# Kernel tuning notes

Measured on AMD Instinct MI355X. Metric: run time of the kernel, lower is better.

## Reference

```python
import jax, jax.numpy as jnp
import numpy as np

N_NODES = 100000
N_EDGES = 1600000
IN_FEATS = 256
N_HIDDEN = 128
N_CLASSES = 40


def setup_inputs() -> dict:
    key = jax.random.key(0)
    k1, k2, k3, k4, k5 = jax.random.split(key, 5)
    features = jax.random.normal(k1, (N_NODES, IN_FEATS), dtype=jnp.float32)
    edge_src = jax.random.randint(k2, (N_EDGES,), 0, N_NODES, dtype=jnp.int64)
    edge_dst = jax.random.randint(k3, (N_EDGES,), 0, N_NODES, dtype=jnp.int64)
    # GraphConv weights (Glorot-ish scaling)
    W1 = jax.random.normal(k4, (IN_FEATS, N_HIDDEN), dtype=jnp.float32) / np.sqrt(IN_FEATS)
    b1 = jnp.zeros((N_HIDDEN,), dtype=jnp.float32)
    W2 = jax.random.normal(k5, (N_HIDDEN, N_CLASSES), dtype=jnp.float32) / np.sqrt(N_HIDDEN)
    b2 = jnpspace = None
    b2 = jnp.zeros((N_CLASSES,), dtype=jnp.float32)
    return {"features": features, "edge_src": edge_src, "edge_dst": edge_dst,
            "W1": W1, "b1": b1, "W2": W2, "b2": b2}


def _degree_norms(edge_src, edge_dst, n_nodes):
    ones = jnp.ones(edge_src.shape[0], dtype=jnp.float32)
    deg_out = jax.ops.segment_sum(ones, edge_src, num_segments=n_nodes)
    deg_in = jax.ops.segment_sum(ones, edge_dst, num_segments=n_nodes)
    norm_src = jax.lax.rsqrt(jnp.clip(deg_out, 1.0))  # D_out^{-1/2}
    norm_dst = jax.lax.rsqrt(jnp.clip(deg_in, 1.0))   # D_in^{-1/2}
    return norm_src, norm_dst


def _graph_conv(x, W, b, edge_src, edge_dst, norm_src, norm_dst, activation=None):
    # DGL GraphConv norm='both': out = D_in^{-1/2} A D_out^{-1/2} (x W) + b
    h = (x @ W) * norm_src[:, None]                       # transform then src-normalize
    agg = jax.ops.segment_sum(h[edge_src], edge_dst,
                              num_segments=x.shape[0])    # sparse neighbor aggregation
    out = agg * norm_dst[:, None] + b
    if activation is not None:
        out = activation(out)
    return out


def reference(features, edge_src, edge_dst, W1, b1, W2, b2):
    norm_src, norm_dst = _degree_norms(edge_src, edge_dst, features.shape[0])
    h = _graph_conv(features, W1, b1, edge_src, edge_dst, norm_src, norm_dst,
                    activation=jax.nn.relu)
    # dropout is identity in eval-mode reference
    out = _graph_conv(h, W2, b2, edge_src, edge_dst, norm_src, norm_dst)
    return out
```

## Files before the change

### kernel.cpp

```cpp
#include <hip/hip_runtime.h>
#include <hip/hip_bf16.h>
#include <hip/hip_fp16.h>

#define NN 100000
#define NE 1600000
#define KF 256
#define NH 128
#define NC 40
#define PAD 64
#define CMAX 63

#define NBLK_P 512
#define PCHUNK (NE / NBLK_P)
#define BUK 256
#define NBUK ((NN + BUK - 1) / BUK)
#define CAP 6144


__device__ __forceinline__ float ldf(const void* p, size_t i, bool bf){
  return bf ? __bfloat162float(((const __hip_bfloat16*)p)[i]) : ((const float*)p)[i];
}
__device__ __forceinline__ void cv2(unsigned int v, float* o){
  union { unsigned int i; float f; } a, b;
  a.i = v << 16; b.i = v & 0xffff0000u;
  o[0] = a.f; o[1] = b.f;
}

__global__ void k_sniff_edges(const unsigned int* __restrict__ e, unsigned int* __restrict__ flags){
  __shared__ unsigned int sh[256];
  unsigned int v = 0;
  for (int i = blockIdx.x * 256 + threadIdx.x; i < NE / 2; i += gridDim.x * 256)
    v |= e[2 * i + 1];
  sh[threadIdx.x] = v;
  __syncthreads();
  for (int off = 128; off; off >>= 1){
    if (threadIdx.x < off) sh[threadIdx.x] |= sh[threadIdx.x + off];
    __syncthreads();
  }
  if (threadIdx.x == 0 && sh[0]) atomicOr(&flags[0], sh[0]);
}

__global__ void k_sniff_float(const unsigned int* __restrict__ w, unsigned int* __restrict__ flags){
  __shared__ unsigned int sh[256];
  unsigned int hits = 0;
  for (int i = blockIdx.x * 256 + threadIdx.x; i < (1 << 20); i += gridDim.x * 256){
    unsigned int b = (w[i] >> 7) & 0xFFu;
    hits += (b >= 118u && b <= 130u) ? 1u : 0u;
  }
  sh[threadIdx.x] = hits;
  __syncthreads();
  for (int off = 128; off; off >>= 1){
    if (threadIdx.x < off) sh[threadIdx.x] += sh[threadIdx.x + off];
    __syncthreads();
  }
  if (threadIdx.x == 0) atomicAdd(&flags[1], sh[0]);
}

__device__ __forceinline__ int edge_at(const void* p, int e, bool is64){
  return is64 ? (int)((const long long*)p)[e] : ((const int*)p)[e];
}
__device__ __forceinline__ bool f_isbf(const unsigned int* flags){ return flags[1] > (1u << 19); }

__global__ __launch_bounds__(256) void k_part(const void* __restrict__ src,
    const void* __restrict__ dst, const unsigned int* __restrict__ flags,
    int* __restrict__ deg_out, int* __restrict__ gcur, unsigned int* __restrict__ part){
  __shared__ int cnt[NBUK];
  __shared__ int base[NBUK];
  const bool is64 = (flags[0] == 0u);
  const int beg = blockIdx.x * PCHUNK;
  const int end = min(beg + PCHUNK, NE);
  for (int t = threadIdx.x; t < NBUK; t += 256) cnt[t] = 0;
  __syncthreads();
  for (int e = beg + threadIdx.x; e < end; e += 256){
    int d = edge_at(dst, e, is64);
    atomicAdd(&cnt[d >> 8], 1);
  }
  __syncthreads();
  for (int t = threadIdx.x; t < NBUK; t += 256){
    int c = cnt[t];
    base[t] = c ? atomicAdd(&gcur[t], c) : 0;
    cnt[t] = 0;
  }
  __syncthreads();
  for (int e = beg + threadIdx.x; e < end; e += 256){
    int d = edge_at(dst, e, is64);
    int s = edge_at(src, e, is64);
    atomicAdd(&deg_out[s], 1);
    int b = d >> 8;
    int pos = base[b] + atomicAdd(&cnt[b], 1);
    if (pos < CAP)
      part[(size_t)b * CAP + pos] = ((unsigned int)s << 8) | (unsigned int)(d & 255);
  }
}

__global__ __launch_bounds__(256) void k_csr(const unsigned int* __restrict__ part,
    const int* __restrict__ gcur, int* __restrict__ fill, int* __restrict__ csr_pad){
  __shared__ int rows[256 * CMAX];
  __shared__ int fl[256];
  const int b = blockIdx.x;
  fl[threadIdx.x] = 0;
  __syncthreads();
  const int n = min(gcur[b], CAP);
  for (int i = threadIdx.x; i < n; i += 256){
    unsigned int e = part[(size_t)b * CAP + i];
    int r = (int)(e & 255u);
    int s = (int)(e >> 8);
    int pos = atomicAdd(&fl[r], 1);
    if (pos < CMAX) rows[r * CMAX + pos] = s;
  }
  __syncthreads();
  const int node0 = b * BUK;
  if (node0 + threadIdx.x < NN) fill[node0 + threadIdx.x] = fl[threadIdx.x];
  for (int idx = threadIdx.x; idx < 256 * CMAX; idx += 256){
    int r = idx / CMAX;
    int c = idx - r * CMAX;
    int node = node0 + r;
    if (node < NN) csr_pad[node * PAD + c] = rows[idx];
  }
}

__global__ void k_norms(const int* __restrict__ deg_out, const int* __restrict__ fill,
                        float* __restrict__ nsrc, float* __restrict__ ndst){
  int i = blockIdx.x * 256 + threadIdx.x;
  if (i < NN){
    nsrc[i] = rsqrtf(fmaxf((float)deg_out[i], 1.f));
    ndst[i] = rsqrtf(fmaxf((float)fill[i], 1.f));
  }
}

__global__ __launch_bounds__(256) void k_gemm1(const void* __restrict__ feat,
    const void* __restrict__ W1, const unsigned int* __restrict__ flags,
    const float* __restrict__ nsrc, __half* __restrict__ h1){
  const bool isbf = f_isbf(flags);
  __shared__ float As[64][68];
  __shared__ float Bs[64][128];
  const int t = threadIdx.x;
  const int row0 = blockIdx.x * 64;
  const int cg = t & 15;
  const int rg = t >> 4;
  float acc[4][8];
  #pragma unroll
  for (int i = 0; i < 4; i++)
    #pragma unroll
    for (int j = 0; j < 8; j++) acc[i][j] = 0.f;

  const int ar   = t >> 2;
  const int ak   = (t & 3) * 16;
  const int arow = row0 + ar;

  for (int kc = 0; kc < KF; kc += 64){
    if (arow < NN){
      size_t off = (size_t)arow * KF + kc + ak;
      if (isbf){
        const uint4* p = (const uint4*)((const __hip_bfloat16*)feat + off);
        uint4 u0 = p[0], u1 = p[1];
        float tmp[16];
        cv2(u0.x, tmp+0);  cv2(u0.y, tmp+2);  cv2(u0.z, tmp+4);  cv2(u0.w, tmp+6);
        cv2(u1.x, tmp+8);  cv2(u1.y, tmp+10); cv2(u1.z, tmp+12); cv2(u1.w, tmp+14);
        #pragma unroll
        for (int j = 0; j < 16; j++) As[ar][ak + j] = tmp[j];
      } else {
        const float4* p = (const float4*)((const float*)feat + off);
        float4 v0 = p[0], v1 = p[1], v2 = p[2], v3 = p[3];
        *(float4*)&As[ar][ak +  0] = v0;
        *(float4*)&As[ar][ak +  4] = v1;
        *(float4*)&As[ar][ak +  8] = v2;
        *(float4*)&As[ar][ak + 12] = v3;
      }
    } else {
      #pragma unroll
      for (int j = 0; j < 16; j++) As[ar][ak + j] = 0.f;
    }
    if (isbf){
      #pragma unroll
      for (int q0 = 0; q0 < 4; q0++){
        int q  = t + q0 * 256;
        int bk = q >> 4;
        int bc = (q & 15) * 8;
        uint4 u = *(const uint4*)((const __hip_bfloat16*)W1 + (size_t)(kc + bk) * NH + bc);
        float tmp[8];
        cv2(u.x, tmp); cv2(u.y, tmp+2); cv2(u.z, tmp+4); cv2(u.w, tmp+6);
        #pragma unroll
        for (int j = 0; j < 8; j++) Bs[bk][bc + j] = tmp[j];
      }
    } else {
      #pragma unroll
      for (int q0 = 0; q0 < 8; q0++){
        int q  = t + q0 * 256;
        int bk = q >> 5;
        int bc = (q & 31) * 4;
        *(float4*)&Bs[bk][bc] = *(const float4*)((const float*)W1 + (size_t)(kc + bk) * NH + bc);
      }
    }
    __syncthreads();
    #pragma unroll 8
    for (int k = 0; k < 64; k++){
      float a0 = As[rg*4+0][k];
      float a1 = As[rg*4+1][k];
      float a2 = As[rg*4+2][k];
      float a3 = As[rg*4+3][k];
      float b[8];
      #pragma unroll
      for (int j = 0; j < 8; j++) b[j] = Bs[k][cg*8 + j];
      #pragma unroll
      for (int j = 0; j < 8; j++){
        acc[0][j] += a0 * b[j];
        acc[1][j] += a1 * b[j];
        acc[2][j] += a2 * b[j];
        acc[3][j] += a3 * b[j];
      }
    }
    __syncthreads();
  }
  #pragma unroll
  for (int i = 0; i < 4; i++){
    int r = row0 + rg*4 + i;
    if (r < NN){
      float s = nsrc[r];
      __half2* op = (__half2*)(h1 + (size_t)r * NH) + cg*4;
      #pragma unroll
      for (int j = 0; j < 4; j++)
        op[j] = __floats2half2_rn(acc[i][2*j] * s, acc[i][2*j+1] * s);
    }
  }
}

__global__ __launch_bounds__(256) void k_agg1(const int* __restrict__ csr_pad,
    const int* __restrict__ fill, const float* __restrict__ ndst,
    const unsigned int* __restrict__ h1w, const void* __restrict__ b1,
    const unsigned int* __restrict__ flags, float* __restrict__ x1){
  const bool isbf = f_isbf(flags);
  int node = blockIdx.x * 4 + (threadIdx.x >> 6);
  if (node >= NN) return;
  int lane = threadIdx.x & 63;
  int beg = node * PAD;
  int end = beg + min(fill[node], CMAX);
  float ax0 = 0.f, ay0 = 0.f, ax1 = 0.f, ay1 = 0.f;
  int e = beg;
  for (; e + 2 <= end; e += 2){
    int s0 = csr_pad[e], s1 = csr_pad[e+1];
    unsigned int u0 = h1w[(size_t)s0 * (NH/2) + lane];
    unsigned int u1 = h1w[(size_t)s1 * (NH/2) + lane];
    float2 v0 = __half22float2(*(__half2*)&u0);
    float2 v1 = __half22float2(*(__half2*)&u1);
    ax0 += v0.x; ay0 += v0.y;
    ax1 += v1.x; ay1 += v1.y;
  }
  if (e < end){
    int s0 = csr_pad[e];
    unsigned int u0 = h1w[(size_t)s0 * (NH/2) + lane];
    float2 v0 = __half22float2(*(__half2*)&u0);
    ax0 += v0.x; ay0 += v0.y;
  }
  float nd = ndst[node];
  float bx = ldf(b1, lane*2,   isbf);
  float by = ldf(b1, lane*2+1, isbf);
  float2 o;
  o.x = fmaxf((ax0 + ax1) * nd + bx, 0.f);
  o.y = fmaxf((ay0 + ay1) * nd + by, 0.f);
  ((float2*)(x1 + (size_t)node * NH))[lane] = o;
}

__global__ __launch_bounds__(256) void k_gemm2(const float* __restrict__ x1,
    const void* __restrict__ W2, const unsigned int* __restrict__ flags,
    const float* __restrict__ nsrc, __half* __restrict__ h2){
  const bool isbf = f_isbf(flags);
  __shared__ float Xs[128][68];
  __shared__ float Ws[64][44];
  const int t = threadIdx.x;
  const int row0 = blockIdx.x * 128;
  const int cg = t & 7;
  const int rg = t >> 3;
  float acc[4][5];
  #pragma unroll
  for (int i = 0; i < 4; i++)
    #pragma unroll
    for (int j = 0; j < 5; j++) acc[i][j] = 0.f;

  for (int kc = 0; kc < NH; kc += 64){
    #pragma unroll
    for (int q0 = 0; q0 < 8; q0++){
      int q  = t + q0 * 256;
      int r  = q >> 4;
      int kq = (q & 15) * 4;
      int grow = row0 + r;
      float4 v;
      if (grow < NN) v = *(const float4*)(x1 + (size_t)grow * NH + kc + kq);
      else { v.x = v.y = v.z = v.w = 0.f; }
      *(float4*)&Xs[r][kq] = v;
    }
    #pragma unroll
    for (int q0 = 0; q0 < 10; q0++){
      int idx = t + q0 * 256;
      int k = idx / 40;
      int c = idx - k * 40;
      Ws[k][c] = ldf(W2, (size_t)(kc + k) * NC + c, isbf);
    }
    __syncthreads();
    #pragma unroll 4
    for (int k = 0; k < 64; k++){
      float a0 = Xs[rg*4+0][k];
      float a1 = Xs[rg*4+1][k];
      float a2 = Xs[rg*4+2][k];
      float a3 = Xs[rg*4+3][k];
      float b[5];
      #pragma unroll
      for (int j = 0; j < 5; j++) b[j] = Ws[k][cg*5 + j];
      #pragma unroll
      for (int j = 0; j < 5; j++){
        acc[0][j] += a0 * b[j];
        acc[1][j] += a1 * b[j];
        acc[2][j] += a2 * b[j];
        acc[3][j] += a3 * b[j];
      }
    }
    __syncthreads();
  }
  #pragma unroll
  for (int i = 0; i < 4; i++){
    int r = row0 + rg*4 + i;
    if (r < NN){
      float s = nsrc[r];
      #pragma unroll
      for (int j = 0; j < 5; j++)
        h2[(size_t)r * NC + cg*5 + j] = __float2half_rn(acc[i][j] * s);
    }
  }
}

__global__ __launch_bounds__(256) void k_agg2(const int* __restrict__ csr_pad,
    const int* __restrict__ fill, const float* __restrict__ ndst,
    const unsigned int* __restrict__ h2w, const void* __restrict__ b2,
    const unsigned int* __restrict__ flags, float* __restrict__ out){
  const bool isbf = f_isbf(flags);
  int node = blockIdx.x * 4 + (threadIdx.x >> 6);
  if (node >= NN) return;
  int lane = threadIdx.x & 63;
  int beg = node * PAD;
  int end = beg + min(fill[node], CMAX);
  if (lane < NC/2){
    float ax0 = 0.f, ay0 = 0.f, ax1 = 0.f, ay1 = 0.f;
    int e = beg;
    for (; e + 2 <= end; e += 2){
      int s0 = csr_pad[e], s1 = csr_pad[e+1];
      unsigned int u0 = h2w[(size_t)s0 * (NC/2) + lane];
      unsigned int u1 = h2w[(size_t)s1 * (NC/2) + lane];
      float2 v0 = __half22float2(*(__half2*)&u0);
      float2 v1 = __half22float2(*(__half2*)&u1);
      ax0 += v0.x; ay0 += v0.y;
      ax1 += v1.x; ay1 += v1.y;
    }
    if (e < end){
      int s0 = csr_pad[e];
      unsigned int u0 = h2w[(size_t)s0 * (NC/2) + lane];
      float2 v0 = __half22float2(*(__half2*)&u0);
      ax0 += v0.x; ay0 += v0.y;
    }
    float nd = ndst[node];
    float2 o;
    o.x = (ax0 + ax1) * nd + ldf(b2, 2*lane,   isbf);
    o.y = (ay0 + ay1) * nd + ldf(b2, 2*lane+1, isbf);
    ((float2*)(out + (size_t)node * NC))[lane] = o;
  }
}

extern "C" void kernel_launch(void* const* d_in, const int* in_sizes, int n_in,
                              void* d_out, int out_size, void* d_ws, size_t ws_size,
                              hipStream_t stream) {
  const long long SZ_FEAT = (long long)NN * KF, SZ_E = NE, SZ_W1 = (long long)KF * NH,
                  SZ_B1 = NH, SZ_W2 = (long long)NH * NC, SZ_B2 = NC;
  int i_feat = -1, i_e1 = -1, i_e2 = -1, i_W1 = -1, i_b1 = -1, i_W2 = -1, i_b2 = -1;
  auto m = [](long long s, long long z){ return s == z || s == 4*z || s == 8*z || s == 2*z; };
  for (int i = 0; i < n_in; i++){
    long long s = in_sizes[i];
    if      (m(s, SZ_FEAT)) i_feat = i;
    else if (m(s, SZ_E))    { if (i_e1 < 0) i_e1 = i; else i_e2 = i; }
    else if (m(s, SZ_W1))   i_W1 = i;
    else if (m(s, SZ_B1))   i_b1 = i;
    else if (m(s, SZ_W2))   i_W2 = i;
    else if (m(s, SZ_B2))   i_b2 = i;
  }
  if (i_feat < 0 || i_e2 < 0 || i_W1 < 0 || i_b1 < 0 || i_W2 < 0 || i_b2 < 0){
    i_feat = 0; i_e1 = 1; i_e2 = 2; i_W1 = 3; i_b1 = 4; i_W2 = 5; i_b2 = 6;
  }
  const void* feat = d_in[i_feat];
  const void* esrc = d_in[i_e1];
  const void* edst = d_in[i_e2];
  const void* W1   = d_in[i_W1];
  const void* b1   = d_in[i_b1];
  const void* W2   = d_in[i_W2];
  const void* b2   = d_in[i_b2];
  float* out = (float*)d_out;

  int* deg_out        = (int*)d_ws;
  int* fill           = deg_out + NN;
  unsigned int* flags = (unsigned int*)(fill + NN);
  int* gcur           = (int*)(flags + 4);
  float* norm_src     = (float*)(gcur + 400);
  float* norm_dst     = norm_src + NN;
  int* csr_pad        = (int*)(norm_dst + NN);
  __half* h1          = (__half*)(csr_pad + (size_t)NN * PAD);
  float* x1           = (float*)(h1 + (size_t)NN * NH);
  __half* h2          = h1;
  unsigned int* part  = (unsigned int*)x1;

  hipMemsetAsync(deg_out, 0, ((size_t)2 * NN + 4 + 400) * sizeof(int), stream);

  k_sniff_edges<<<400, 256, 0, stream>>>((const unsigned int*)esrc, flags);
  k_sniff_float<<<256, 256, 0, stream>>>((const unsigned int*)feat, flags);
  k_part<<<NBLK_P, 256, 0, stream>>>(esrc, edst, flags, deg_out, gcur, part);
  k_csr <<<NBUK,   256, 0, stream>>>(part, gcur, fill, csr_pad);
  k_norms<<<(NN + 255) / 256, 256, 0, stream>>>(deg_out, fill, norm_src, norm_dst);

  k_gemm1<<<(NN + 63) / 64, 256, 0, stream>>>(feat, W1, flags, norm_src, h1);
  k_agg1 <<<(NN + 3) / 4, 256, 0, stream>>>(csr_pad, fill, norm_dst,
                                            (const unsigned int*)h1, b1, flags, x1);
  k_gemm2<<<(NN + 127) / 128, 256, 0, stream>>>(x1, W2, flags, norm_src, h2);
  k_agg2 <<<(NN + 3) / 4, 256, 0, stream>>>(csr_pad, fill, norm_dst,
                                            (const unsigned int*)h2, b2, flags, out);
}
```

Measured before the change: 599.6 us.

## Add bf16 MFMA path for first-layer GEMM with pre-swizzled weights

Adds a kernel that rearranges W1 into per-lane bf16x8 fragments, plus a new GEMM1 kernel that uses 16x16x32 bf16 MFMA instructions when the inputs are detected as bf16. The old shared-memory scalar GEMM1 now handles only the fp32 case. The aim is to replace scalar FMA work and bf16-to-float conversion with matrix-core instructions. The cost is two extra kernel launches: the weight swizzle, and whichever GEMM kernel exits early for the other dtype.

Result: no change. 594.2 us (-0.9%).

```diff
diff --git a/kernel.cpp b/kernel.cpp
--- a/kernel.cpp
+++ b/kernel.cpp
@@ -15,6 +15,9 @@
 #define BUK 256
 #define NBUK ((NN + BUK - 1) / BUK)
 #define CAP 6144
+
+typedef __attribute__((ext_vector_type(8))) short bf16x8;
+typedef __attribute__((ext_vector_type(4))) float f32x4;
 
 
 __device__ __forceinline__ float ldf(const void* p, size_t i, bool bf){
@@ -128,10 +131,68 @@
   }
 }
 
+__global__ void k_w1s(const void* __restrict__ W1, const unsigned int* __restrict__ flags,
+                      bf16x8* __restrict__ w1s){
+  if (!f_isbf(flags)) return;
+  int idx = blockIdx.x * 256 + threadIdx.x;
+  if (idx >= 4096) return;
+  int l    = idx & 63;
+  int tile = idx >> 6;
+  int kt   = tile >> 3;
+  int nt   = tile & 7;
+  int krow = kt * 32 + (l >> 4) * 8;
+  int col  = nt * 16 + (l & 15);
+  const unsigned short* w = (const unsigned short*)W1;
+  bf16x8 v;
+  #pragma unroll
+  for (int j = 0; j < 8; j++)
+    v[j] = (short)w[(size_t)(krow + j) * NH + col];
+  w1s[idx] = v;
+}
+
+__global__ __launch_bounds__(256) void k_gemm1_mfma(const void* __restrict__ feat,
+    const bf16x8* __restrict__ w1s, const unsigned int* __restrict__ flags,
+    const float* __restrict__ nsrc, __half* __restrict__ h1){
+  if (!f_isbf(flags)) return;
+  const int t  = threadIdx.x;
+  const int wv = t >> 6;
+  const int l  = t & 63;
+  const int row0 = blockIdx.x * 64 + wv * 16;
+  const int arow = row0 + (l & 15);
+  const short* fp = (const short*)feat;
+  const size_t abase = (size_t)min(arow, NN - 1) * KF + (l >> 4) * 8;
+
+  f32x4 acc[8];
+  #pragma unroll
+  for (int n = 0; n < 8; n++) acc[n] = (f32x4){0.f, 0.f, 0.f, 0.f};
+
+  #pragma unroll 2
+  for (int kt = 0; kt < 8; kt++){
+    bf16x8 a = *(const bf16x8*)(fp + abase + kt * 32);
+    #pragma unroll
+    for (int n = 0; n < 8; n++){
+      bf16x8 b = w1s[(kt * 8 + n) * 64 + l];
+      acc[n] = __builtin_amdgcn_mfma_f32_16x16x32_bf16(a, b, acc[n], 0, 0, 0);
+    }
+  }
+  const int rbase = row0 + (l >> 4) * 4;
+  const int col   = l & 15;
+  #pragma unroll
+  for (int i = 0; i < 4; i++){
+    int r = rbase + i;
+    if (r < NN){
+      float s = nsrc[r];
+      #pragma unroll
+      for (int n = 0; n < 8; n++)
+        h1[(size_t)r * NH + n * 16 + col] = __float2half_rn(acc[n][i] * s);
+    }
+  }
+}
+
 __global__ __launch_bounds__(256) void k_gemm1(const void* __restrict__ feat,
     const void* __restrict__ W1, const unsigned int* __restrict__ flags,
     const float* __restrict__ nsrc, __half* __restrict__ h1){
-  const bool isbf = f_isbf(flags);
+  if (f_isbf(flags)) return;
   __shared__ float As[64][68];
   __shared__ float Bs[64][128];
   const int t = threadIdx.x;
@@ -151,46 +212,22 @@
   for (int kc = 0; kc < KF; kc += 64){
     if (arow < NN){
       size_t off = (size_t)arow * KF + kc + ak;
-      if (isbf){
-        const uint4* p = (const uint4*)((const __hip_bfloat16*)feat + off);
-        uint4 u0 = p[0], u1 = p[1];
-        float tmp[16];
-        cv2(u0.x, tmp+0);  cv2(u0.y, tmp+2);  cv2(u0.z, tmp+4);  cv2(u0.w, tmp+6);
-        cv2(u1.x, tmp+8);  cv2(u1.y, tmp+10); cv2(u1.z, tmp+12); cv2(u1.w, tmp+14);
-        #pragma unroll
-        for (int j = 0; j < 16; j++) As[ar][ak + j] = tmp[j];
-      } else {
-        const float4* p = (const float4*)((const float*)feat + off);
-        float4 v0 = p[0], v1 = p[1], v2 = p[2], v3 = p[3];
-        *(float4*)&As[ar][ak +  0] = v0;
-        *(float4*)&As[ar][ak +  4] = v1;
-        *(float4*)&As[ar][ak +  8] = v2;
-        *(float4*)&As[ar][ak + 12] = v3;
-      }
+      const float4* p = (const float4*)((const float*)feat + off);
+      float4 v0 = p[0], v1 = p[1], v2 = p[2], v3 = p[3];
+      *(float4*)&As[ar][ak +  0] = v0;
+      *(float4*)&As[ar][ak +  4] = v1;
+      *(float4*)&As[ar][ak +  8] = v2;
+      *(float4*)&As[ar][ak + 12] = v3;
     } else {
       #pragma unroll
       for (int j = 0; j < 16; j++) As[ar][ak + j] = 0.f;
     }
-    if (isbf){
-      #pragma unroll
-      for (int q0 = 0; q0 < 4; q0++){
-        int q  = t + q0 * 256;
-        int bk = q >> 4;
-        int bc = (q & 15) * 8;
-        uint4 u = *(const uint4*)((const __hip_bfloat16*)W1 + (size_t)(kc + bk) * NH + bc);
-        float tmp[8];
-        cv2(u.x, tmp); cv2(u.y, tmp+2); cv2(u.z, tmp+4); cv2(u.w, tmp+6);
-        #pragma unroll
-        for (int j = 0; j < 8; j++) Bs[bk][bc + j] = tmp[j];
-      }
-    } else {
-      #pragma unroll
-      for (int q0 = 0; q0 < 8; q0++){
-        int q  = t + q0 * 256;
-        int bk = q >> 5;
-        int bc = (q & 31) * 4;
-        *(float4*)&Bs[bk][bc] = *(const float4*)((const float*)W1 + (size_t)(kc + bk) * NH + bc);
-      }
+    #pragma unroll
+    for (int q0 = 0; q0 < 8; q0++){
+      int q  = t + q0 * 256;
+      int bk = q >> 5;
+      int bc = (q & 31) * 4;
+      *(float4*)&Bs[bk][bc] = *(const float4*)((const float*)W1 + (size_t)(kc + bk) * NH + bc);
     }
     __syncthreads();
     #pragma unroll 8
@@ -403,16 +440,19 @@
   float* x1           = (float*)(h1 + (size_t)NN * NH);
   __half* h2          = h1;
   unsigned int* part  = (unsigned int*)x1;
+  bf16x8* w1s         = (bf16x8*)((char*)x1 + (16u << 20));
 
   hipMemsetAsync(deg_out, 0, ((size_t)2 * NN + 4 + 400) * sizeof(int), stream);
 
   k_sniff_edges<<<400, 256, 0, stream>>>((const unsigned int*)esrc, flags);
   k_sniff_float<<<256, 256, 0, stream>>>((const unsigned int*)feat, flags);
+  k_w1s <<<16, 256, 0, stream>>>(W1, flags, w1s);
   k_part<<<NBLK_P, 256, 0, stream>>>(esrc, edst, flags, deg_out, gcur, part);
   k_csr <<<NBUK,   256, 0, stream>>>(part, gcur, fill, csr_pad);
   k_norms<<<(NN + 255) / 256, 256, 0, stream>>>(deg_out, fill, norm_src, norm_dst);
 
-  k_gemm1<<<(NN + 63) / 64, 256, 0, stream>>>(feat, W1, flags, norm_src, h1);
+  k_gemm1     <<<(NN + 63) / 64, 256, 0, stream>>>(feat, W1, flags, norm_src, h1);
+  k_gemm1_mfma<<<(NN + 63) / 64, 256, 0, stream>>>(feat, w1s, flags, norm_src, h1);
   k_agg1 <<<(NN + 3) / 4, 256, 0, stream>>>(csr_pad, fill, norm_dst,
                                             (const unsigned int*)h1, b1, flags, x1);
   k_gemm2<<<(NN + 127) / 128, 256, 0, stream>>>(x1, W2, flags, norm_src, h2);
```
